# Optimization experiments

Hardware: AMD Instinct MI355X
Metric: run time of the kernel (lower is better)

## Reference

```python
import jax, jax.numpy as jnp
import numpy as np

N_NODES = 100000
N_EDGES = 1600000
D_IN = 64
D_OUT = 64
BN_EPS = 1e-5


def setup_inputs() -> dict:
    key = jax.random.key(0)
    k1, k2, k3 = jax.random.split(key, 3)
    x = jax.random.normal(k1, (N_NODES, D_IN), dtype=jnp.float32)
    edge_index = jax.random.randint(k2, (2, N_EDGES), 0, N_NODES, dtype=jnp.int64)
    # GCNConv linear weight [out, in], glorot-ish scale
    W = jax.random.normal(k3, (D_OUT, D_IN), dtype=jnp.float32) / np.sqrt(D_IN)
    b = jnp.zeros((D_OUT,), dtype=jnp.float32)
    gamma = jnp.ones((D_OUT,), dtype=jnp.float32)
    beta = jnp.zeros((D_OUT,), dtype=jnp.float32)
    return {"x": x, "edge_index": edge_index, "W": W, "b": b, "gamma": gamma, "beta": beta}


def reference(x, edge_index, W, b, gamma, beta):
    # --- GCNConv: h = x @ W^T, propagate with sym-normalized adjacency + self-loops ---
    h = x @ W.T  # [N, D_OUT]
    src, tgt = edge_index[0], edge_index[1]
    # degree at target nodes, +1 for self-loop
    deg = jax.ops.segment_sum(jnp.ones((src.shape[0],), h.dtype), tgt,
                              num_segments=N_NODES) + 1.0  # [N]
    dinv = jax.lax.rsqrt(deg)
    norm = dinv[src] * dinv[tgt]  # [E]
    # gather -> scale -> scatter-add; self-loop contribution is h / deg
    agg = jax.ops.segment_sum(h[src] * norm[:, None], tgt, num_segments=N_NODES)
    out = agg + h * (1.0 / deg)[:, None] + b  # [N, D_OUT]
    # --- BatchNorm1d (training-mode batch statistics, biased variance) ---
    mean = out.mean(axis=0)
    var = out.var(axis=0)
    y = gamma * (out - mean) * jax.lax.rsqrt(var + BN_EPS) + beta
    # --- ReLU (dropout = identity in eval) ---
    return jax.nn.relu(y)
```

## Files before the change

kernel.cpp:

```cpp
#include <hip/hip_runtime.h>
#include <stdint.h>

#define N_NODES_C 100000
#define N_EDGES_C 1600000
#define DIM 64
#define BN_EPS_C 1e-5f
#define BSH 7
#define NB 782
#define CH 6144

__device__ __forceinline__ int ld_idx(const void* p, int is64, size_t i) {
    if (is64) return (int)((const long long*)p)[i];
    return ((const int*)p)[i];
}

__device__ __forceinline__ int probe_is64(const unsigned int* __restrict__ p) {
    int lane = threadIdx.x & 63;
    unsigned int v = (lane < 32) ? p[2 * lane + 1] : 0u;
    return __ballot(v != 0u) == 0ull;
}

__global__ __launch_bounds__(1024) void hist_kernel(const void* __restrict__ ei,
                                                    int* __restrict__ bucket_cnt) {
    __shared__ int hist[NB];
    for (int i = threadIdx.x; i < NB; i += 1024) hist[i] = 0;
    __syncthreads();
    int is64 = probe_is64((const unsigned int*)ei);
    int stride = gridDim.x * blockDim.x;
    for (int e = blockIdx.x * blockDim.x + threadIdx.x; e < N_EDGES_C; e += stride) {
        int tg = ld_idx(ei, is64, (size_t)N_EDGES_C + e);
        atomicAdd(&hist[tg >> BSH], 1);
    }
    __syncthreads();
    for (int i = threadIdx.x; i < NB; i += 1024) {
        int c = hist[i];
        if (c) atomicAdd(&bucket_cnt[i], c);
    }
}

__global__ __launch_bounds__(1024) void bucketscan_kernel(const int* __restrict__ bucket_cnt,
                                                          int* __restrict__ bucket_base,
                                                          int* __restrict__ bucket_cursor) {
    __shared__ int s[1024];
    int t = threadIdx.x;
    int v = (t < NB) ? bucket_cnt[t] : 0;
    s[t] = v;
    __syncthreads();
    for (int off = 1; off < 1024; off <<= 1) {
        int u = (t >= off) ? s[t - off] : 0;
        __syncthreads();
        s[t] += u;
        __syncthreads();
    }
    if (t < NB) {
        int excl = s[t] - v;
        bucket_base[t] = excl;
        bucket_cursor[t] = excl;
    }
}

__global__ __launch_bounds__(1024) void binscatter_kernel(const void* __restrict__ ei,
                                                          int* __restrict__ bucket_cursor,
                                                          unsigned int* __restrict__ csr) {
    __shared__ int hist[NB];
    __shared__ int base[NB];
    int is64 = probe_is64((const unsigned int*)ei);
    int e0 = blockIdx.x * CH;
    int eend = min(e0 + CH, N_EDGES_C);
    for (int i = threadIdx.x; i < NB; i += 1024) hist[i] = 0;
    __syncthreads();
    for (int e = e0 + threadIdx.x; e < eend; e += 1024) {
        int tg = ld_idx(ei, is64, (size_t)N_EDGES_C + e);
        atomicAdd(&hist[tg >> BSH], 1);
    }
    __syncthreads();
    for (int i = threadIdx.x; i < NB; i += 1024) {
        int c = hist[i];
        base[i] = c ? atomicAdd(&bucket_cursor[i], c) : 0;
        hist[i] = 0;
    }
    __syncthreads();
    for (int e = e0 + threadIdx.x; e < eend; e += 1024) {
        int s  = ld_idx(ei, is64, (size_t)e);
        int tg = ld_idx(ei, is64, (size_t)N_EDGES_C + e);
        int b  = tg >> BSH;
        int tl = tg & 127;
        int pos = base[b] + atomicAdd(&hist[b], 1);
        csr[pos] = ((unsigned int)tl << 17) | (unsigned int)s;
    }
}

__global__ __launch_bounds__(256) void sort_kernel(const unsigned int* __restrict__ csr,
                                                   const int* __restrict__ bucket_base,
                                                   const int* __restrict__ bucket_cnt,
                                                   int* __restrict__ csr2,
                                                   int* __restrict__ rowbase,
                                                   float* __restrict__ dinv) {
    __shared__ int cnt[128];
    __shared__ int sbase[129];
    __shared__ int cur[128];
    int bk = blockIdx.x;
    int t = threadIdx.x;
    if (t < 128) cnt[t] = 0;
    __syncthreads();
    int base = bucket_base[bk], n = bucket_cnt[bk];
    for (int i = t; i < n; i += 256) {
        atomicAdd(&cnt[csr[base + i] >> 17], 1);
    }
    __syncthreads();
    if (t == 0) {
        int run = 0;
        for (int k = 0; k < 128; ++k) { sbase[k] = run; run += cnt[k]; }
        sbase[128] = run;
    }
    __syncthreads();
    if (t < 128) {
        cur[t] = base + sbase[t];
        int node = (bk << BSH) + t;
        if (node < N_NODES_C) {
            rowbase[node] = base + sbase[t];
            dinv[node] = rsqrtf((float)(cnt[t] + 1));
        }
    }
    if (bk == 0 && t == 0) rowbase[N_NODES_C] = N_EDGES_C;
    __syncthreads();
    for (int i = t; i < n; i += 256) {
        unsigned int v = csr[base + i];
        int tl = v >> 17;
        int pos = atomicAdd(&cur[tl], 1);
        csr2[pos] = (int)(v & 0x1FFFF);
    }
}

__global__ __launch_bounds__(256) void gemm_kernel(const float* __restrict__ x,
                                                   const float* __restrict__ W,
                                                   const float* __restrict__ dinv,
                                                   signed char* __restrict__ hs8,
                                                   float* __restrict__ scale) {
    __shared__ float Wl[DIM * 65];
    __shared__ float xs[32][DIM];
    int t = threadIdx.x;
    for (int i = t; i < DIM * DIM; i += 256) {
        Wl[(i >> 6) * 65 + (i & 63)] = W[i];
    }
    int r0 = blockIdx.x * 32;
    for (int i = t; i < 32 * DIM; i += 256) {
        int row = i >> 6, col = i & 63;
        int r = r0 + row;
        xs[row][col] = (r < N_NODES_C) ? x[(size_t)r * DIM + col] : 0.0f;
    }
    __syncthreads();
    int wv = t >> 6, c = t & 63;
    float acc[8];
#pragma unroll
    for (int it = 0; it < 8; ++it) acc[it] = 0.0f;
    for (int k = 0; k < DIM; ++k) {
        float w = Wl[c * 65 + k];
#pragma unroll
        for (int it = 0; it < 8; ++it)
            acc[it] = fmaf(xs[it * 4 + wv][k], w, acc[it]);
    }
#pragma unroll
    for (int it = 0; it < 8; ++it) {
        int r = r0 + it * 4 + wv;
        if (r < N_NODES_C) {
            float v = acc[it] * dinv[r];
            float m = fabsf(v);
#pragma unroll
            for (int off = 32; off >= 1; off >>= 1)
                m = fmaxf(m, __shfl_xor(m, off, 64));
            float inv = (m > 0.0f) ? 127.0f / m : 0.0f;
            int q = (int)rintf(v * inv);
            hs8[(size_t)r * DIM + c] = (signed char)q;
            if (c == 0) scale[r] = m * (1.0f / 127.0f);
        }
    }
}

__global__ __launch_bounds__(256) void gather_kernel(const int* __restrict__ csr2,
                                                     const int* __restrict__ rowbase,
                                                     const float* __restrict__ dinv,
                                                     const unsigned short* __restrict__ hsu,
                                                     const float* __restrict__ scale,
                                                     const float* __restrict__ b_,
                                                     float2* __restrict__ out,
                                                     float* __restrict__ sums,
                                                     float* __restrict__ sumsq) {
    int lane = threadIdx.x & 63;
    int half = lane >> 5;
    int c2 = lane & 31;
    int wid = blockIdx.x * (blockDim.x >> 6) + (threadIdx.x >> 6);
    int nw = gridDim.x * (blockDim.x >> 6);
    float2 bb = ((const float2*)b_)[c2];
    float s0a = 0.0f, q0a = 0.0f, s1a = 0.0f, q1a = 0.0f;

#define ISSUE8(BUF, KB)                                                        \
    _Pragma("unroll")                                                          \
    for (int k = 0; k < 8; ++k) {                                              \
        int s = __shfl(idxv, (KB) + k, 32);                                    \
        BUF[k] = (unsigned int)hsu[(size_t)s * 32 + c2];                       \
    }
#define CONSUME8(BUF, KB)                                                      \
    _Pragma("unroll")                                                          \
    for (int k = 0; k < 8; ++k) {                                              \
        bool use = ((KB) + k) < nl;                                            \
        float sc = __shfl(sclv, (KB) + k, 32);                                 \
        float scm = use ? sc : 0.0f;                                           \
        float q0 = (float)(int)(signed char)(BUF[k] & 0xFF);                   \
        float q1 = (float)(int)(signed char)(BUF[k] >> 8);                     \
        a0 = fmaf(q0, scm, a0);                                                \
        a1 = fmaf(q1, scm, a1);                                                \
    }

    for (int p = wid; p < N_NODES_C / 2; p += nw) {
        int t = 2 * p + half;
        int base = rowbase[t];
        int end = rowbase[t + 1];
        int n = end - base;
        int n_oth = __shfl_xor(n, 32, 64);
        int nmax = max(n, n_oth);
        float a0 = 0.0f, a1 = 0.0f;
        for (int kd = 0; kd < nmax; kd += 32) {
            int nl = n - kd;
            int off = (nl > 0) ? min(c2, nl - 1) : 0;
            int pos = min(base + kd + off, N_EDGES_C - 1);
            int idxv = __builtin_nontemporal_load(&csr2[pos]);
            float sclv = scale[idxv];
            int nml = min(nmax - kd, 32);
            unsigned int uA[8], uB[8];
            ISSUE8(uA, 0);
            if (nml > 8)  { ISSUE8(uB, 8); }
            CONSUME8(uA, 0);
            if (nml > 16) { ISSUE8(uA, 16); }
            if (nml > 8)  { CONSUME8(uB, 8); }
            if (nml > 24) { ISSUE8(uB, 24); }
            if (nml > 16) { CONSUME8(uA, 16); }
            if (nml > 24) { CONSUME8(uB, 24); }
        }
        unsigned int ut = (unsigned int)hsu[(size_t)t * 32 + c2];
        float sct = scale[t];
        float qt0 = (float)(int)(signed char)(ut & 0xFF);
        float qt1 = (float)(int)(signed char)(ut >> 8);
        a0 = fmaf(qt0, sct, a0);
        a1 = fmaf(qt1, sct, a1);
        float dt = dinv[t];
        a0 = fmaf(a0, dt, bb.x);
        a1 = fmaf(a1, dt, bb.y);
        union { float2 f; unsigned long long u; } cvt;
        cvt.f = make_float2(a0, a1);
        __builtin_nontemporal_store(cvt.u,
            (unsigned long long*)&out[(size_t)t * 32 + c2]);
        s0a += a0; q0a += a0 * a0;
        s1a += a1; q1a += a1 * a1;
    }
#undef ISSUE8
#undef CONSUME8

    __shared__ float r0[256], r1[256], r2[256], r3[256];
    r0[threadIdx.x] = s0a; r1[threadIdx.x] = q0a;
    r2[threadIdx.x] = s1a; r3[threadIdx.x] = q1a;
    __syncthreads();
    if (threadIdx.x < 32) {
        float S0 = 0, Q0 = 0, S1 = 0, Q1 = 0;
        for (int k = threadIdx.x; k < 256; k += 32) {
            S0 += r0[k]; Q0 += r1[k]; S1 += r2[k]; Q1 += r3[k];
        }
        unsafeAtomicAdd(&sums[2 * threadIdx.x], S0);
        unsafeAtomicAdd(&sums[2 * threadIdx.x + 1], S1);
        unsafeAtomicAdd(&sumsq[2 * threadIdx.x], Q0);
        unsafeAtomicAdd(&sumsq[2 * threadIdx.x + 1], Q1);
    }
}

__global__ __launch_bounds__(256) void bnrelu_kernel(float4* __restrict__ out,
                                                     const float* __restrict__ sums,
                                                     const float* __restrict__ sumsq,
                                                     const float* __restrict__ gamma,
                                                     const float* __restrict__ beta) {
    __shared__ float sc[DIM], sh[DIM];
    int t = threadIdx.x;
    if (t < DIM) {
        float m = sums[t] * (1.0f / N_NODES_C);
        float var = sumsq[t] * (1.0f / N_NODES_C) - m * m;
        float s = gamma[t] * rsqrtf(var + BN_EPS_C);
        sc[t] = s;
        sh[t] = beta[t] - m * s;
    }
    __syncthreads();
    const int n4 = N_NODES_C * (DIM / 4);
    int stride = gridDim.x * blockDim.x;
    for (int i = blockIdx.x * blockDim.x + t; i < n4; i += stride) {
        int cb = (i & 15) * 4;
        float4 v = out[i];
        v.x = fmaxf(fmaf(v.x, sc[cb + 0], sh[cb + 0]), 0.0f);
        v.y = fmaxf(fmaf(v.y, sc[cb + 1], sh[cb + 1]), 0.0f);
        v.z = fmaxf(fmaf(v.z, sc[cb + 2], sh[cb + 2]), 0.0f);
        v.w = fmaxf(fmaf(v.w, sc[cb + 3], sh[cb + 3]), 0.0f);
        out[i] = v;
    }
}

extern "C" void kernel_launch(void* const* d_in, const int* in_sizes, int n_in,
                              void* d_out, int out_size, void* d_ws, size_t ws_size,
                              hipStream_t stream) {
    const float* x     = (const float*)d_in[0];
    const void*  ei    = d_in[1];
    const float* W     = (const float*)d_in[2];
    const float* b     = (const float*)d_in[3];
    const float* gamma = (const float*)d_in[4];
    const float* beta  = (const float*)d_in[5];
    float* out = (float*)d_out;

    char* ws = (char*)d_ws;
    int*   bucket_cnt    = (int*)(ws + 256);
    int*   bucket_base   = (int*)(ws + 3584);
    int*   bucket_cursor = (int*)(ws + 6912);
    float* dinv          = (float*)(ws + 10240);
    int*   rowbase       = (int*)(ws + 410240);
    float* sums          = (float*)(ws + 810496);
    float* sumsq         = (float*)(ws + 810752);
    float* scale         = (float*)(ws + 811008);
    unsigned int* csr    = (unsigned int*)(ws + 1211264);
    int*   csr2          = (int*)(ws + 7611264);
    signed char* hs8     = (signed char*)(ws + 14011264);

    hipMemsetAsync(bucket_cnt, 0, NB * sizeof(int), stream);
    hipMemsetAsync(sums, 0, 512, stream);

    hist_kernel<<<256, 1024, 0, stream>>>(ei, bucket_cnt);
    bucketscan_kernel<<<1, 1024, 0, stream>>>(bucket_cnt, bucket_base, bucket_cursor);
    binscatter_kernel<<<(N_EDGES_C + CH - 1) / CH, 1024, 0, stream>>>(ei, bucket_cursor, csr);
    sort_kernel<<<NB, 256, 0, stream>>>(csr, bucket_base, bucket_cnt, csr2,
                                        rowbase, dinv);
    gemm_kernel<<<(N_NODES_C + 31) / 32, 256, 0, stream>>>(x, W, dinv, hs8, scale);
    gather_kernel<<<2048, 256, 0, stream>>>(csr2, rowbase, dinv,
                                            (const unsigned short*)hs8, scale, b,
                                            (float2*)out, sums, sumsq);
    bnrelu_kernel<<<1024, 256, 0, stream>>>((float4*)out, sums, sumsq, gamma, beta);
}
```

Before: 231.2 us.

## Pack per-edge source scale into CSR entries and compute degrees via global atomics

Reorders the pipeline so the GEMM/quantize runs first with an unnormalized per-row scale. Degrees are then counted with global atomics in the histogram pass, and a small kernel folds dinv into that scale. The sort kernel writes (src, scale) pairs into the CSR, so the gather reads the scale alongside the index instead of doing a dependent random load. In exchange it adds 1.6M global atomics, a memset and an extra kernel, and doubles the size of the CSR array the gather reads.

```diff
diff --git a/kernel.cpp b/kernel.cpp
--- a/kernel.cpp
+++ b/kernel.cpp
@@ -20,8 +20,53 @@
     return __ballot(v != 0u) == 0ull;
 }
 
-__global__ __launch_bounds__(1024) void hist_kernel(const void* __restrict__ ei,
-                                                    int* __restrict__ bucket_cnt) {
+__global__ __launch_bounds__(256) void gemm_kernel(const float* __restrict__ x,
+                                                   const float* __restrict__ W,
+                                                   signed char* __restrict__ hs8,
+                                                   float* __restrict__ scomb) {
+    __shared__ float Wl[DIM * 65];
+    __shared__ float xs[32][DIM];
+    int t = threadIdx.x;
+    for (int i = t; i < DIM * DIM; i += 256) {
+        Wl[(i >> 6) * 65 + (i & 63)] = W[i];
+    }
+    int r0 = blockIdx.x * 32;
+    for (int i = t; i < 32 * DIM; i += 256) {
+        int row = i >> 6, col = i & 63;
+        int r = r0 + row;
+        xs[row][col] = (r < N_NODES_C) ? x[(size_t)r * DIM + col] : 0.0f;
+    }
+    __syncthreads();
+    int wv = t >> 6, c = t & 63;
+    float acc[8];
+#pragma unroll
+    for (int it = 0; it < 8; ++it) acc[it] = 0.0f;
+    for (int k = 0; k < DIM; ++k) {
+        float w = Wl[c * 65 + k];
+#pragma unroll
+        for (int it = 0; it < 8; ++it)
+            acc[it] = fmaf(xs[it * 4 + wv][k], w, acc[it]);
+    }
+#pragma unroll
+    for (int it = 0; it < 8; ++it) {
+        int r = r0 + it * 4 + wv;
+        if (r < N_NODES_C) {
+            float v = acc[it];
+            float m = fabsf(v);
+#pragma unroll
+            for (int off = 32; off >= 1; off >>= 1)
+                m = fmaxf(m, __shfl_xor(m, off, 64));
+            float inv = (m > 0.0f) ? 127.0f / m : 0.0f;
+            int q = (int)rintf(v * inv);
+            hs8[(size_t)r * DIM + c] = (signed char)q;
+            if (c == 0) scomb[r] = m * (1.0f / 127.0f);
+        }
+    }
+}
+
+__global__ __launch_bounds__(1024) void histdeg_kernel(const void* __restrict__ ei,
+                                                       int* __restrict__ bucket_cnt,
+                                                       int* __restrict__ deg) {
     __shared__ int hist[NB];
     for (int i = threadIdx.x; i < NB; i += 1024) hist[i] = 0;
     __syncthreads();
@@ -30,6 +75,7 @@
     for (int e = blockIdx.x * blockDim.x + threadIdx.x; e < N_EDGES_C; e += stride) {
         int tg = ld_idx(ei, is64, (size_t)N_EDGES_C + e);
         atomicAdd(&hist[tg >> BSH], 1);
+        atomicAdd(&deg[tg], 1);
     }
     __syncthreads();
     for (int i = threadIdx.x; i < NB; i += 1024) {
@@ -56,6 +102,17 @@
         int excl = s[t] - v;
         bucket_base[t] = excl;
         bucket_cursor[t] = excl;
+    }
+}
+
+__global__ __launch_bounds__(256) void dinvscomb_kernel(const int* __restrict__ deg,
+                                                        float* __restrict__ dinv,
+                                                        float* __restrict__ scomb) {
+    int i = blockIdx.x * blockDim.x + threadIdx.x;
+    if (i < N_NODES_C) {
+        float di = rsqrtf((float)(deg[i] + 1));
+        dinv[i] = di;
+        scomb[i] *= di;
     }
 }
 
@@ -90,12 +147,12 @@
     }
 }
 
-__global__ __launch_bounds__(256) void sort_kernel(const unsigned int* __restrict__ csr,
-                                                   const int* __restrict__ bucket_base,
-                                                   const int* __restrict__ bucket_cnt,
-                                                   int* __restrict__ csr2,
-                                                   int* __restrict__ rowbase,
-                                                   float* __restrict__ dinv) {
+__global__ __launch_bounds__(256) void sortq_kernel(const unsigned int* __restrict__ csr,
+                                                    const int* __restrict__ bucket_base,
+                                                    const int* __restrict__ bucket_cnt,
+                                                    const float* __restrict__ scomb,
+                                                    uint2* __restrict__ csr2q,
+                                                    int* __restrict__ rowbase) {
     __shared__ int cnt[128];
     __shared__ int sbase[129];
     __shared__ int cur[128];
@@ -117,71 +174,24 @@
     if (t < 128) {
         cur[t] = base + sbase[t];
         int node = (bk << BSH) + t;
-        if (node < N_NODES_C) {
-            rowbase[node] = base + sbase[t];
-            dinv[node] = rsqrtf((float)(cnt[t] + 1));
-        }
+        if (node < N_NODES_C) rowbase[node] = base + sbase[t];
     }
     if (bk == 0 && t == 0) rowbase[N_NODES_C] = N_EDGES_C;
     __syncthreads();
     for (int i = t; i < n; i += 256) {
         unsigned int v = csr[base + i];
         int tl = v >> 17;
+        int src = (int)(v & 0x1FFFF);
         int pos = atomicAdd(&cur[tl], 1);
-        csr2[pos] = (int)(v & 0x1FFFF);
-    }
-}
-
-__global__ __launch_bounds__(256) void gemm_kernel(const float* __restrict__ x,
-                                                   const float* __restrict__ W,
-                                                   const float* __restrict__ dinv,
-                                                   signed char* __restrict__ hs8,
-                                                   float* __restrict__ scale) {
-    __shared__ float Wl[DIM * 65];
-    __shared__ float xs[32][DIM];
-    int t = threadIdx.x;
-    for (int i = t; i < DIM * DIM; i += 256) {
-        Wl[(i >> 6) * 65 + (i & 63)] = W[i];
-    }
-    int r0 = blockIdx.x * 32;
-    for (int i = t; i < 32 * DIM; i += 256) {
-        int row = i >> 6, col = i & 63;
-        int r = r0 + row;
-        xs[row][col] = (r < N_NODES_C) ? x[(size_t)r * DIM + col] : 0.0f;
-    }
-    __syncthreads();
-    int wv = t >> 6, c = t & 63;
-    float acc[8];
-#pragma unroll
-    for (int it = 0; it < 8; ++it) acc[it] = 0.0f;
-    for (int k = 0; k < DIM; ++k) {
-        float w = Wl[c * 65 + k];
-#pragma unroll
-        for (int it = 0; it < 8; ++it)
-            acc[it] = fmaf(xs[it * 4 + wv][k], w, acc[it]);
-    }
-#pragma unroll
-    for (int it = 0; it < 8; ++it) {
-        int r = r0 + it * 4 + wv;
-        if (r < N_NODES_C) {
-            float v = acc[it] * dinv[r];
-            float m = fabsf(v);
-#pragma unroll
-            for (int off = 32; off >= 1; off >>= 1)
-                m = fmaxf(m, __shfl_xor(m, off, 64));
-            float inv = (m > 0.0f) ? 127.0f / m : 0.0f;
-            int q = (int)rintf(v * inv);
-            hs8[(size_t)r * DIM + c] = (signed char)q;
-            if (c == 0) scale[r] = m * (1.0f / 127.0f);
-        }
-    }
-}
-
-__global__ __launch_bounds__(256) void gather_kernel(const int* __restrict__ csr2,
+        csr2q[pos] = make_uint2((unsigned int)src, __float_as_uint(scomb[src]));
+    }
+}
+
+__global__ __launch_bounds__(256) void gather_kernel(const uint2* __restrict__ csr2q,
                                                      const int* __restrict__ rowbase,
                                                      const float* __restrict__ dinv,
                                                      const unsigned short* __restrict__ hsu,
-                                                     const float* __restrict__ scale,
+                                                     const float* __restrict__ scomb,
                                                      const float* __restrict__ b_,
                                                      float2* __restrict__ out,
                                                      float* __restrict__ sums,
@@ -224,8 +234,10 @@
             int nl = n - kd;
             int off = (nl > 0) ? min(c2, nl - 1) : 0;
             int pos = min(base + kd + off, N_EDGES_C - 1);
-            int idxv = __builtin_nontemporal_load(&csr2[pos]);
-            float sclv = scale[idxv];
+            unsigned long long vv = __builtin_nontemporal_load(
+                (const unsigned long long*)&csr2q[pos]);
+            int idxv = (int)(unsigned int)(vv & 0xFFFFFFFFull);
+            float sclv = __uint_as_float((unsigned int)(vv >> 32));
             int nml = min(nmax - kd, 32);
             unsigned int uA[8], uB[8];
             ISSUE8(uA, 0);
@@ -238,7 +250,7 @@
             if (nml > 24) { CONSUME8(uB, 24); }
         }
         unsigned int ut = (unsigned int)hsu[(size_t)t * 32 + c2];
-        float sct = scale[t];
+        float sct = scomb[t];
         float qt0 = (float)(int)(signed char)(ut & 0xFF);
         float qt1 = (float)(int)(signed char)(ut >> 8);
         a0 = fmaf(qt0, sct, a0);
@@ -316,25 +328,28 @@
     int*   bucket_base   = (int*)(ws + 3584);
     int*   bucket_cursor = (int*)(ws + 6912);
     float* dinv          = (float*)(ws + 10240);
-    int*   rowbase       = (int*)(ws + 410240);
-    float* sums          = (float*)(ws + 810496);
-    float* sumsq         = (float*)(ws + 810752);
-    float* scale         = (float*)(ws + 811008);
-    unsigned int* csr    = (unsigned int*)(ws + 1211264);
-    int*   csr2          = (int*)(ws + 7611264);
-    signed char* hs8     = (signed char*)(ws + 14011264);
+    int*   deg_rowbase   = (int*)(ws + 410240);
+    float* sums          = (float*)(ws + 810304);
+    float* sumsq         = (float*)(ws + 810560);
+    float* scomb         = (float*)(ws + 810816);
+    unsigned int* csr    = (unsigned int*)(ws + 1210880);
+    uint2* csr2q         = (uint2*)(ws + 7610880);
+    signed char* hs8     = (signed char*)(ws + 20410880);
 
     hipMemsetAsync(bucket_cnt, 0, NB * sizeof(int), stream);
+    hipMemsetAsync(deg_rowbase, 0, (size_t)N_NODES_C * sizeof(int), stream);
     hipMemsetAsync(sums, 0, 512, stream);
 
-    hist_kernel<<<256, 1024, 0, stream>>>(ei, bucket_cnt);
+    gemm_kernel<<<(N_NODES_C + 31) / 32, 256, 0, stream>>>(x, W, hs8, scomb);
+    histdeg_kernel<<<256, 1024, 0, stream>>>(ei, bucket_cnt, deg_rowbase);
     bucketscan_kernel<<<1, 1024, 0, stream>>>(bucket_cnt, bucket_base, bucket_cursor);
+    dinvscomb_kernel<<<(N_NODES_C + 255) / 256, 256, 0, stream>>>(deg_rowbase,
+                                                                  dinv, scomb);
     binscatter_kernel<<<(N_EDGES_C + CH - 1) / CH, 1024, 0, stream>>>(ei, bucket_cursor, csr);
-    sort_kernel<<<NB, 256, 0, stream>>>(csr, bucket_base, bucket_cnt, csr2,
-                                        rowbase, dinv);
-    gemm_kernel<<<(N_NODES_C + 31) / 32, 256, 0, stream>>>(x, W, dinv, hs8, scale);
-    gather_kernel<<<2048, 256, 0, stream>>>(csr2, rowbase, dinv,
-                                            (const unsigned short*)hs8, scale, b,
+    sortq_kernel<<<NB, 256, 0, stream>>>(csr, bucket_base, bucket_cnt, scomb,
+                                         csr2q, deg_rowbase);
+    gather_kernel<<<2048, 256, 0, stream>>>(csr2q, deg_rowbase, dinv,
+                                            (const unsigned short*)hs8, scomb, b,
                                             (float2*)out, sums, sumsq);
     bnrelu_kernel<<<1024, 256, 0, stream>>>((float4*)out, sums, sumsq, gamma, beta);
 }
```

Result: slower. 302.4 us (+30.8%).
